# Kernel optimization log

Hardware: AMD Instinct MI355X
Metric: run time of the kernel (lower is better)

Reference implementation:

```python
import jax, jax.numpy as jnp
import numpy as np

B, S, H = 1024, 100, 256          # users(batch), seq_len, hidden
L, U = 20000, 20000               # location_size, user_size
EL, EU = 500000, 400000           # nnz of loc-loc and user-loc sparse graphs
LAMBDA_T, LAMBDA_S = 0.1, 1000.0
DAY = 86400.0


def setup_inputs() -> dict:
    key = jax.random.key(0)
    k = jax.random.split(key, 20)
    sd = 1.0 / np.sqrt(H)
    full_seq = jax.random.randint(k[0], (B, S), 0, L)
    full_seq_map = jax.random.randint(k[1], (B, S), 0, L)
    length = jax.random.randint(k[2], (B,), 1, S + 1)  # >=1 so mask never empty
    user_id = jax.random.randint(k[3], (B,), 0, U)
    time_delta = jax.random.uniform(k[4], (B, S), dtype=jnp.float32) * DAY
    geo_delta = jax.random.uniform(k[5], (B, S), dtype=jnp.float32) * 1e-3
    enc_emb = jax.random.normal(k[6], (L, H), dtype=jnp.float32) * sd
    user_emb = jax.random.normal(k[7], (U, H), dtype=jnp.float32) * sd
    emb2 = jax.random.normal(k[8], (L, H), dtype=jnp.float32) * sd  # embed_layer table
    # loc-loc random-walk graph (row-normalized weights), COO edge list
    row_loc = jax.random.randint(k[9], (EL,), 0, L)
    col_loc = jax.random.randint(k[10], (EL,), 0, L)
    vals_loc = jax.random.uniform(k[11], (EL,), dtype=jnp.float32) / (EL / L)
    # user-loc interact graph (row-normalized), COO edge list
    row_usr = jax.random.randint(k[12], (EU,), 0, U)
    col_usr = jax.random.randint(k[13], (EU,), 0, L)
    vals_usr = jax.random.uniform(k[14], (EU,), dtype=jnp.float32) / (EU / U)
    W_ih = jax.random.normal(k[15], (H, H), dtype=jnp.float32) * sd
    W_hh = jax.random.normal(k[16], (H, H), dtype=jnp.float32) * sd
    b_ih = jnp.zeros((H,), jnp.float32)
    b_hh = jnp.zeros((H,), jnp.float32)
    W1 = jax.random.normal(k[17], (L, 3 * H), dtype=jnp.float32) * sd  # source declares 2H but feeds 3H concat
    b1 = jnp.zeros((L,), jnp.float32)
    h0 = jax.random.normal(k[18], (B, H), dtype=jnp.float32) * (1.0 / H)  # per-user random init state
    return dict(full_seq=full_seq, full_seq_map=full_seq_map, length=length,
                user_id=user_id, time_delta=time_delta, geo_delta=geo_delta,
                enc_emb=enc_emb, user_emb=user_emb, emb2=emb2,
                row_loc=row_loc, col_loc=col_loc, vals_loc=vals_loc,
                row_usr=row_usr, col_usr=col_usr, vals_usr=vals_usr,
                W_ih=W_ih, W_hh=W_hh, b_ih=b_ih, b_hh=b_hh, W1=W1, b1=b1, h0=h0)


def reference(full_seq, full_seq_map, length, user_id, time_delta, geo_delta,
              enc_emb, user_emb, emb2, row_loc, col_loc, vals_loc,
              row_usr, col_usr, vals_usr, W_ih, W_hh, b_ih, b_hh, W1, b1, h0):
    # sparse.mm(graph, loc_emb): one random-walk propagation over locations
    encoder_weight = jax.ops.segment_sum(vals_loc[:, None] * enc_emb[col_loc],
                                         row_loc, num_segments=L)  # [L,H]
    x_emb = encoder_weight[full_seq_map]                           # [B,S,H]
    # sparse.mm(interact_graph, loc_emb): user preference from visited locations
    ew_user = jax.ops.segment_sum(vals_usr[:, None] * enc_emb[col_usr],
                                  row_usr, num_segments=U)         # [U,H]
    user_pref = ew_user[user_id][:, None, :]                       # [B,1,H]
    user_loc_sim = jnp.exp(-jnp.linalg.norm(user_pref - x_emb, axis=-1))  # [B,S]
    # vanilla tanh RNN (batch_first), scan over time
    def step(h, x_t):
        h = jnp.tanh(x_t @ W_ih.T + b_ih + h @ W_hh.T + b_hh)
        return h, h
    _, outs = jax.lax.scan(step, h0, jnp.swapaxes(x_emb, 0, 1))    # [S,B,H]
    out = jnp.swapaxes(outs, 0, 1)                                 # [B,S,H]
    # temporal / spatial decay weights
    a_j = (jnp.cos(time_delta * 2 * np.pi / DAY) + 1) / 2 * jnp.exp(-(time_delta / DAY * LAMBDA_T))
    b_j = jnp.exp(-geo_delta * LAMBDA_S)
    w_j = (a_j * b_j + 1e-10) * user_loc_sim
    mask = (length[:, None] > jnp.arange(S)[None, :]).astype(w_j.dtype)
    w_j = w_j * mask                                               # [B,S]
    denom = jnp.sum(w_j, axis=1, keepdims=True)                    # [B,1]
    out_w = jnp.sum(out * w_j[..., None], axis=1) / denom          # [B,H]
    x2 = emb2[full_seq]                                            # embed_layer (dropout=eval)
    out_w2 = jnp.sum(x2 * w_j[..., None], axis=1) / denom          # [B,H]
    p_u = user_emb[user_id]                                        # [B,H]
    feat = jnp.concatenate([out_w, p_u, out_w2], axis=1)           # [B,3H]
    return feat @ W1.T + b1                                        # [B,L]
```

## Files before the change

### kernel.cpp

```cpp
#include <hip/hip_runtime.h>
#include <math.h>

#define B_  1024
#define S_  100
#define H_  256
#define L_  20000
#define U_  20000
#define EL_ 500000
#define EU_ 400000

typedef __bf16 bf16x8 __attribute__((ext_vector_type(8)));
typedef __bf16 bf16x4 __attribute__((ext_vector_type(4)));
typedef float  f32x4  __attribute__((ext_vector_type(4)));
typedef _Float16 f16x8 __attribute__((ext_vector_type(8)));

__global__ void k_mark(const int* __restrict__ uid, int* __restrict__ flags) {
    int i = blockIdx.x * blockDim.x + threadIdx.x;
    if (i < B_) flags[uid[i]] = 1;
}

__global__ void k_hist2(const int* __restrict__ rowL, const int* __restrict__ rowU,
                        const int* __restrict__ flags,
                        int* __restrict__ cntL, int* __restrict__ cntU) {
    int e = blockIdx.x * blockDim.x + threadIdx.x;
    if (e < EL_) {
        atomicAdd(&cntL[rowL[e]], 1);
    } else if (e < EL_ + EU_) {
        int r = rowU[e - EL_];
        if (flags[r]) atomicAdd(&cntU[r], 1);
    }
}

__global__ __launch_bounds__(1024) void k_scan2(const int* __restrict__ cntA,
                                                int* __restrict__ offsA, int* __restrict__ curA,
                                                const int* __restrict__ cntB,
                                                int* __restrict__ offsB, int* __restrict__ curB) {
    const int* cnt = blockIdx.x ? cntB : cntA;
    int* offs      = blockIdx.x ? offsB : offsA;
    int* cursor    = blockIdx.x ? curB : curA;
    __shared__ int wsum[16];
    __shared__ int carry_s;
    int tid = threadIdx.x;
    int lane = tid & 63, wv = tid >> 6;
    if (tid == 0) carry_s = 0;
    __syncthreads();
    for (int base = 0; base < L_; base += 1024) {
        int v = (base + tid < L_) ? cnt[base + tid] : 0;
        int x = v;
#pragma unroll
        for (int off = 1; off < 64; off <<= 1) {
            int y = __shfl_up(x, off, 64);
            if (lane >= off) x += y;
        }
        if (lane == 63) wsum[wv] = x;
        __syncthreads();
        if (wv == 0) {
            int s = (lane < 16) ? wsum[lane] : 0;
#pragma unroll
            for (int off = 1; off < 16; off <<= 1) {
                int y = __shfl_up(s, off, 64);
                if (lane >= off) s += y;
            }
            if (lane < 16) wsum[lane] = s;
        }
        __syncthreads();
        int excl = x - v + (wv ? wsum[wv - 1] : 0) + carry_s;
        if (base + tid < L_) { offs[base + tid] = excl; cursor[base + tid] = excl; }
        __syncthreads();
        if (tid == 0) carry_s += wsum[15];
        __syncthreads();
    }
    if (tid == 0) offs[L_] = carry_s;
}

__global__ void k_place2(const int* __restrict__ rowL, const int* __restrict__ colL,
                         const float* __restrict__ valL, int* __restrict__ curL,
                         int* __restrict__ colLs, float* __restrict__ valLs,
                         const int* __restrict__ rowU, const int* __restrict__ colU,
                         const float* __restrict__ valU, const int* __restrict__ flags,
                         int* __restrict__ curU, int* __restrict__ colUs,
                         float* __restrict__ valUs) {
    int e = blockIdx.x * blockDim.x + threadIdx.x;
    if (e < EL_) {
        int pos = atomicAdd(&curL[rowL[e]], 1);
        colLs[pos] = colL[e];
        valLs[pos] = valL[e];
    } else if (e < EL_ + EU_) {
        int e2 = e - EL_;
        int r = rowU[e2];
        if (!flags[r]) return;
        int pos = atomicAdd(&curU[r], 1);
        colUs[pos] = colU[e2];
        valUs[pos] = valU[e2];
    }
}

__global__ __launch_bounds__(256) void k_gather2(
        const int* __restrict__ offsL, const int* __restrict__ colLs,
        const float* __restrict__ valLs, float* __restrict__ encw,
        const int* __restrict__ offsU, const int* __restrict__ colUs,
        const float* __restrict__ valUs, float* __restrict__ ewu,
        const int* __restrict__ flags, const float* __restrict__ emb) {
    int r = blockIdx.x;
    const int* offs; const int* col_s; const float* val_s; float* out;
    if (r < L_) {
        offs = offsL; col_s = colLs; val_s = valLs; out = encw;
    } else {
        r -= L_;
        if (!flags[r]) return;
        offs = offsU; col_s = colUs; val_s = valUs; out = ewu;
    }
    int tid = threadIdx.x;
    int lo = offs[r], hi = offs[r + 1];
    float acc = 0.f;
    int i = lo;
    for (; i + 1 < hi; i += 2) {
        int c0 = col_s[i], c1 = col_s[i + 1];
        float v0 = val_s[i], v1 = val_s[i + 1];
        float e0 = emb[(long long)c0 * H_ + tid];
        float e1 = emb[(long long)c1 * H_ + tid];
        acc += v0 * e0 + v1 * e1;
    }
    if (i < hi) acc += val_s[i] * emb[(long long)col_s[i] * H_ + tid];
    out[(long long)r * H_ + tid] = acc;
}

#define BM 128
#define BN 128
#define BK 16
#define PADW 132

__global__ __launch_bounds__(256) void k_gemm(
        const float* __restrict__ A, const float* __restrict__ Bm,
        const float* __restrict__ bias1, const float* __restrict__ bias2,
        float* __restrict__ C, int M, int N, int K) {
    __shared__ float As[BK][PADW];
    __shared__ float Bs[BK][PADW];
    int m0 = blockIdx.x * BM;
    int n0 = blockIdx.y * BN;
    int tid = threadIdx.x;
    int tn = tid & 15, tm = tid >> 4;

    float acc[8][8];
#pragma unroll
    for (int i = 0; i < 8; i++)
#pragma unroll
        for (int j = 0; j < 8; j++) acc[i][j] = 0.f;

    for (int k0 = 0; k0 < K; k0 += BK) {
#pragma unroll
        for (int h = 0; h < 2; h++) {
            int v = tid + h * 256;
            int rw = v >> 2, c4 = v & 3;
            int ar = m0 + rw; if (ar > M - 1) ar = M - 1;
            float4 a = *(const float4*)(A + (long long)ar * K + k0 + c4 * 4);
            As[c4 * 4 + 0][rw] = a.x; As[c4 * 4 + 1][rw] = a.y;
            As[c4 * 4 + 2][rw] = a.z; As[c4 * 4 + 3][rw] = a.w;
            int br = n0 + rw; if (br > N - 1) br = N - 1;
            float4 b = *(const float4*)(Bm + (long long)br * K + k0 + c4 * 4);
            Bs[c4 * 4 + 0][rw] = b.x; Bs[c4 * 4 + 1][rw] = b.y;
            Bs[c4 * 4 + 2][rw] = b.z; Bs[c4 * 4 + 3][rw] = b.w;
        }
        __syncthreads();
#pragma unroll
        for (int kk = 0; kk < BK; kk++) {
            float4 a0 = *(const float4*)&As[kk][tm * 8];
            float4 a1 = *(const float4*)&As[kk][tm * 8 + 4];
            float4 b0 = *(const float4*)&Bs[kk][tn * 8];
            float4 b1 = *(const float4*)&Bs[kk][tn * 8 + 4];
            float av[8] = {a0.x, a0.y, a0.z, a0.w, a1.x, a1.y, a1.z, a1.w};
            float bv[8] = {b0.x, b0.y, b0.z, b0.w, b1.x, b1.y, b1.z, b1.w};
#pragma unroll
            for (int i = 0; i < 8; i++)
#pragma unroll
                for (int j = 0; j < 8; j++) acc[i][j] += av[i] * bv[j];
        }
        __syncthreads();
    }

    float bsum[8];
#pragma unroll
    for (int j = 0; j < 8; j++) {
        int n = n0 + tn * 8 + j;
        float bb = 0.f;
        if (n < N) {
            if (bias1) bb += bias1[n];
            if (bias2) bb += bias2[n];
        }
        bsum[j] = bb;
    }
#pragma unroll
    for (int i = 0; i < 8; i++) {
        int m = m0 + tm * 8 + i;
        if (m < M) {
#pragma unroll
            for (int j = 0; j < 8; j++) {
                int n = n0 + tn * 8 + j;
                if (n < N) C[(long long)m * N + n] = acc[i][j] + bsum[j];
            }
        }
    }
}

__global__ __launch_bounds__(256) void k_cvt(const float4* __restrict__ src,
                                             bf16x4* __restrict__ dst, int n4) {
    int i = blockIdx.x * blockDim.x + threadIdx.x;
    if (i >= n4) return;
    float4 v = src[i];
    bf16x4 o;
    o[0] = (__bf16)v.x; o[1] = (__bf16)v.y; o[2] = (__bf16)v.z; o[3] = (__bf16)v.w;
    dst[i] = o;
}

__global__ __launch_bounds__(256) void k_gemm_bf16(
        const __bf16* __restrict__ A, const __bf16* __restrict__ Bw,
        const float* __restrict__ bias, float* __restrict__ C,
        int M, int N, int K) {
    __shared__ __bf16 Asl[128 * 32];
    __shared__ __bf16 Bsl[128 * 32];
    int tid = threadIdx.x;
    int lane = tid & 63, w = tid >> 6;
    int wm = w >> 1, wn = w & 1;
    int m0 = blockIdx.x * 128, n0 = blockIdx.y * 128;

    f32x4 acc[4][4];
#pragma unroll
    for (int i = 0; i < 4; i++)
#pragma unroll
        for (int j = 0; j < 4; j++) acc[i][j] = (f32x4){0.f, 0.f, 0.f, 0.f};

    int fm = lane & 15, fq = lane >> 4;

    for (int k0 = 0; k0 < K; k0 += 32) {
#pragma unroll
        for (int h = 0; h < 2; h++) {
            int c = h * 256 + w * 64 + lane;
            int r = c >> 2, qsw = c & 3;
            int q = qsw ^ ((r >> 1) & 3);
            const __bf16* gA = A + (long long)(m0 + r) * K + k0 + q * 8;
            __builtin_amdgcn_global_load_lds(
                (const __attribute__((address_space(1))) void*)gA,
                (__attribute__((address_space(3))) void*)(Asl + (h * 256 + w * 64) * 8),
                16, 0, 0);
            int br = n0 + r; if (br > N - 1) br = N - 1;
            const __bf16* gB = Bw + (long long)br * K + k0 + q * 8;
            __builtin_amdgcn_global_load_lds(
                (const __attribute__((address_space(1))) void*)gB,
                (__attribute__((address_space(3))) void*)(Bsl + (h * 256 + w * 64) * 8),
                16, 0, 0);
        }
        __syncthreads();

        bf16x8 af[4], bfr[4];
#pragma unroll
        for (int mi = 0; mi < 4; mi++) {
            int r = wm * 64 + mi * 16 + fm;
            int ch = r * 4 + (fq ^ ((r >> 1) & 3));
            af[mi] = *(const bf16x8*)(Asl + ch * 8);
        }
#pragma unroll
        for (int ni = 0; ni < 4; ni++) {
            int r = wn * 64 + ni * 16 + fm;
            int ch = r * 4 + (fq ^ ((r >> 1) & 3));
            bfr[ni] = *(const bf16x8*)(Bsl + ch * 8);
        }
#pragma unroll
        for (int mi = 0; mi < 4; mi++)
#pragma unroll
            for (int ni = 0; ni < 4; ni++)
                acc[mi][ni] = __builtin_amdgcn_mfma_f32_16x16x32_bf16(
                    af[mi], bfr[ni], acc[mi][ni], 0, 0, 0);
        __syncthreads();
    }

#pragma unroll
    for (int ni = 0; ni < 4; ni++) {
        int col = n0 + wn * 64 + ni * 16 + fm;
        if (col >= N) continue;
        float bb = bias[col];
#pragma unroll
        for (int mi = 0; mi < 4; mi++) {
            int row = m0 + wm * 64 + mi * 16 + fq * 4;
#pragma unroll
            for (int r = 0; r < 4; r++)
                C[(long long)(row + r) * N + col] = acc[mi][ni][r] + bb;
        }
    }
}

__global__ __launch_bounds__(256) void k_simwj(
        const int* __restrict__ map, const int* __restrict__ length, const int* __restrict__ uid,
        const float* __restrict__ td_, const float* __restrict__ gd_,
        const float* __restrict__ encw, const float* __restrict__ ewu,
        float* __restrict__ wj, float* __restrict__ denom) {
    int b = blockIdx.x;
    __shared__ float up[H_];
    __shared__ float wjl[S_];
    int tid = threadIdx.x;
    int u = uid[b];
    up[tid] = ewu[(long long)u * H_ + tid];
    __syncthreads();
    int wv = tid >> 6, lane = tid & 63;
    int len = length[b];
    for (int s = wv; s < S_; s += 4) {
        int mi = map[b * S_ + s];
        float4 x = ((const float4*)(encw + (long long)mi * H_))[lane];
        float4 uu = *(const float4*)&up[lane * 4];
        float dx = uu.x - x.x, dy = uu.y - x.y, dz = uu.z - x.z, dw = uu.w - x.w;
        float d2 = dx * dx + dy * dy + dz * dz + dw * dw;
#pragma unroll
        for (int off = 32; off; off >>= 1) d2 += __shfl_xor(d2, off, 64);
        if (lane == 0) {
            float nrm = sqrtf(d2);
            float sim = expf(-nrm);
            float td = td_[b * S_ + s], gd = gd_[b * S_ + s];
            float aj = (cosf(td * 7.27220521664304e-05f) + 1.0f) * 0.5f *
                       expf(-td * 1.1574074074074073e-06f);
            float bj = expf(-gd * 1000.0f);
            float w = (aj * bj + 1e-10f) * sim;
            if (s >= len) w = 0.f;
            wjl[s] = w;
            wj[b * S_ + s] = w;
        }
    }
    __syncthreads();
    if (tid < 64) {
        float v = (tid < S_) ? wjl[tid] : 0.f;
        if (tid + 64 < S_) v += wjl[tid + 64];
#pragma unroll
        for (int off = 32; off; off >>= 1) v += __shfl_xor(v, off, 64);
        if (tid == 0) denom[b] = v;
    }
}

#define RNN_STRIDE 264

__global__ __launch_bounds__(512, 1) void k_rnn_mfma(
        const float* __restrict__ EWW, const float* __restrict__ Whh,
        const int* __restrict__ map, const float* __restrict__ wj,
        const float* __restrict__ h0g, float* __restrict__ out_acc) {
    __shared__ _Float16 hbuf[16 * RNN_STRIDE];
    __shared__ int   maps_s[S_ * 16];
    __shared__ float wjs_s[S_ * 16];

    int tid = threadIdx.x;
    int lane = tid & 63, w = tid >> 6;
    int fm = lane & 15, fq = lane >> 4;
    int b0 = blockIdx.x * 16;

    for (int i = tid; i < 16 * S_; i += 512) {
        int m = i / S_, s = i - m * S_;
        maps_s[s * 16 + m] = map[(b0 + m) * S_ + s];
        wjs_s[s * 16 + m] = wj[(b0 + m) * S_ + s];
    }
    if (tid < 256) {
        int m = tid >> 4, seg = tid & 15;
        const float4* src = (const float4*)(h0g + (long long)(b0 + m) * H_ + seg * 16);
        float4 a = src[0], bq = src[1], cq = src[2], dq = src[3];
        f16x8 v0, v1;
        v0[0] = (_Float16)a.x;  v0[1] = (_Float16)a.y;  v0[2] = (_Float16)a.z;  v0[3] = (_Float16)a.w;
        v0[4] = (_Float16)bq.x; v0[5] = (_Float16)bq.y; v0[6] = (_Float16)bq.z; v0[7] = (_Float16)bq.w;
        v1[0] = (_Float16)cq.x; v1[1] = (_Float16)cq.y; v1[2] = (_Float16)cq.z; v1[3] = (_Float16)cq.w;
        v1[4] = (_Float16)dq.x; v1[5] = (_Float16)dq.y; v1[6] = (_Float16)dq.z; v1[7] = (_Float16)dq.w;
        *(f16x8*)(hbuf + m * RNN_STRIDE + seg * 16) = v0;
        *(f16x8*)(hbuf + m * RNN_STRIDE + seg * 16 + 8) = v1;
    }

    f16x8 wf[2][8];
#pragma unroll
    for (int ni = 0; ni < 2; ni++) {
        const float* wrow = Whh + (long long)(w * 32 + ni * 16 + fm) * H_;
#pragma unroll
        for (int c = 0; c < 8; c++) {
            int k = c * 32 + fq * 8;
            float4 p = *(const float4*)(wrow + k);
            float4 q = *(const float4*)(wrow + k + 4);
            f16x8 v;
            v[0] = (_Float16)p.x; v[1] = (_Float16)p.y; v[2] = (_Float16)p.z; v[3] = (_Float16)p.w;
            v[4] = (_Float16)q.x; v[5] = (_Float16)q.y; v[6] = (_Float16)q.z; v[7] = (_Float16)q.w;
            wf[ni][c] = v;
        }
    }

    float accv[2][4];
#pragma unroll
    for (int ni = 0; ni < 2; ni++)
#pragma unroll
        for (int r = 0; r < 4; r++) accv[ni][r] = 0.f;

    __syncthreads();

    float xc[2][4], xn[2][4];
#pragma unroll
    for (int r = 0; r < 4; r++) {
        const float* xp = EWW + (long long)maps_s[0 * 16 + fq * 4 + r] * H_;
#pragma unroll
        for (int ni = 0; ni < 2; ni++) xc[ni][r] = xp[w * 32 + ni * 16 + fm];
    }

    for (int s = 0; s < S_; s++) {
        f32x4 acc[2];
#pragma unroll
        for (int ni = 0; ni < 2; ni++)
            acc[ni] = (f32x4){xc[ni][0], xc[ni][1], xc[ni][2], xc[ni][3]};

        if (s + 1 < S_) {
#pragma unroll
            for (int r = 0; r < 4; r++) {
                const float* xp = EWW + (long long)maps_s[(s + 1) * 16 + fq * 4 + r] * H_;
#pragma unroll
                for (int ni = 0; ni < 2; ni++) xn[ni][r] = xp[w * 32 + ni * 16 + fm];
            }
        }

        f16x8 af[8];
#pragma unroll
        for (int c = 0; c < 8; c++)
            af[c] = *(const f16x8*)(hbuf + fm * RNN_STRIDE + c * 32 + fq * 8);
#pragma unroll
        for (int c = 0; c < 8; c++)
#pragma unroll
            for (int ni = 0; ni < 2; ni++)
                acc[ni] = __builtin_amdgcn_mfma_f32_16x16x32_f16(af[c], wf[ni][c], acc[ni], 0, 0, 0);
        __syncthreads();

        float wjr[4];
#pragma unroll
        for (int r = 0; r < 4; r++) wjr[r] = wjs_s[s * 16 + fq * 4 + r];
#pragma unroll
        for (int ni = 0; ni < 2; ni++) {
#pragma unroll
            for (int r = 0; r < 4; r++) {
                float t = acc[ni][r];
                t = fminf(15.f, fmaxf(-15.f, t));
                float e = __expf(2.f * t);
                float hv = 1.f - 2.f / (e + 1.f);
                accv[ni][r] += wjr[r] * hv;
                hbuf[(fq * 4 + r) * RNN_STRIDE + w * 32 + ni * 16 + fm] = (_Float16)hv;
            }
        }
        __syncthreads();

#pragma unroll
        for (int ni = 0; ni < 2; ni++)
#pragma unroll
            for (int r = 0; r < 4; r++) xc[ni][r] = xn[ni][r];
    }

#pragma unroll
    for (int ni = 0; ni < 2; ni++)
#pragma unroll
        for (int r = 0; r < 4; r++)
            out_acc[(long long)(b0 + fq * 4 + r) * H_ + w * 32 + ni * 16 + fm] = accv[ni][r];
}

__global__ __launch_bounds__(256) void k_feat(
        const float* __restrict__ out_acc, const float* __restrict__ denom,
        const int* __restrict__ uid, const float* __restrict__ user_emb,
        const int* __restrict__ seq, const float* __restrict__ wj,
        const float* __restrict__ emb2, float* __restrict__ feat) {
    int b = blockIdx.x, j = threadIdx.x;
    __shared__ float wjl[S_];
    __shared__ int sq[S_];
    if (j < S_) {
        wjl[j] = wj[b * S_ + j];
        sq[j] = seq[b * S_ + j];
    }
    __syncthreads();
    float inv = 1.f / denom[b];
    feat[(long long)b * 768 + j] = out_acc[(long long)b * H_ + j] * inv;
    feat[(long long)b * 768 + 256 + j] = user_emb[(long long)uid[b] * H_ + j];
    float a2 = 0.f;
    for (int s = 0; s < S_; s++) a2 += wjl[s] * emb2[(long long)sq[s] * H_ + j];
    feat[(long long)b * 768 + 512 + j] = a2 * inv;
}

extern "C" void kernel_launch(void* const* d_in, const int* in_sizes, int n_in,
                              void* d_out, int out_size, void* d_ws, size_t ws_size,
                              hipStream_t stream) {
    const int*   full_seq     = (const int*)d_in[0];
    const int*   full_seq_map = (const int*)d_in[1];
    const int*   length       = (const int*)d_in[2];
    const int*   user_id      = (const int*)d_in[3];
    const float* time_delta   = (const float*)d_in[4];
    const float* geo_delta    = (const float*)d_in[5];
    const float* enc_emb      = (const float*)d_in[6];
    const float* user_emb     = (const float*)d_in[7];
    const float* emb2         = (const float*)d_in[8];
    const int*   row_loc      = (const int*)d_in[9];
    const int*   col_loc      = (const int*)d_in[10];
    const float* vals_loc     = (const float*)d_in[11];
    const int*   row_usr      = (const int*)d_in[12];
    const int*   col_usr      = (const int*)d_in[13];
    const float* vals_usr     = (const float*)d_in[14];
    const float* W_ih         = (const float*)d_in[15];
    const float* W_hh         = (const float*)d_in[16];
    const float* b_ih         = (const float*)d_in[17];
    const float* b_hh         = (const float*)d_in[18];
    const float* W1           = (const float*)d_in[19];
    const float* b1           = (const float*)d_in[20];
    const float* h0g          = (const float*)d_in[21];
    float* out = (float*)d_out;

    float* ws = (float*)d_ws;
    size_t o = 0;
    int*   flags = (int*)(ws + o); o += U_;
    float* ewu   = ws + o; o += (size_t)U_ * H_;
    float* encw  = ws + o; o += (size_t)L_ * H_;
    float* EWW   = ws + o; o += (size_t)L_ * H_;
    size_t late_base = o;
    float* wj    = ws + o; o += (size_t)B_ * S_;
    float* denom = ws + o; o += B_;
    float* oacc  = ws + o; o += (size_t)B_ * H_;
    float* feat  = ws + o; o += (size_t)B_ * 3 * H_;
    size_t a = late_base;
    int*   cntL  = (int*)(ws + a); a += L_ + 1;
    int*   offsL = (int*)(ws + a); a += L_ + 1;
    int*   curL  = (int*)(ws + a); a += L_ + 1;
    int*   colLs = (int*)(ws + a); a += EL_;
    float* valLs = ws + a;         a += EL_;
    int*   cntU  = (int*)EWW;
    int*   offsU = cntU + (U_ + 1);
    int*   curU  = offsU + (U_ + 1);
    int*   colUs = curU + (U_ + 1);
    float* valUs = (float*)(colUs + EU_);
    __bf16* w1bf   = (__bf16*)ws;
    __bf16* featbf = (__bf16*)EWW;

    hipMemsetAsync(flags, 0, U_ * sizeof(int), stream);
    hipMemsetAsync(cntL, 0, (L_ + 1) * sizeof(int), stream);
    hipMemsetAsync(cntU, 0, (U_ + 1) * sizeof(int), stream);
    k_mark<<<(B_ + 255) / 256, 256, 0, stream>>>(user_id, flags);

    k_hist2<<<(EL_ + EU_ + 255) / 256, 256, 0, stream>>>(row_loc, row_usr, flags, cntL, cntU);
    k_scan2<<<2, 1024, 0, stream>>>(cntL, offsL, curL, cntU, offsU, curU);
    k_place2<<<(EL_ + EU_ + 255) / 256, 256, 0, stream>>>(
        row_loc, col_loc, vals_loc, curL, colLs, valLs,
        row_usr, col_usr, vals_usr, flags, curU, colUs, valUs);
    k_gather2<<<L_ + U_, 256, 0, stream>>>(offsL, colLs, valLs, encw,
                                           offsU, colUs, valUs, ewu, flags, enc_emb);

    k_gemm<<<dim3((L_ + BM - 1) / BM, (H_ + BN - 1) / BN), 256, 0, stream>>>(
        encw, W_ih, b_ih, b_hh, EWW, L_, H_, H_);
    k_simwj<<<B_, 256, 0, stream>>>(full_seq_map, length, user_id, time_delta,
                                    geo_delta, encw, ewu, wj, denom);
    k_rnn_mfma<<<B_ / 16, 512, 0, stream>>>(EWW, W_hh, full_seq_map, wj, h0g, oacc);
    k_feat<<<B_, 256, 0, stream>>>(oacc, denom, user_id, user_emb, full_seq, wj, emb2, feat);

    k_cvt<<<((L_ * 3 * H_ / 4) + 255) / 256, 256, 0, stream>>>(
        (const float4*)W1, (bf16x4*)w1bf, L_ * 3 * H_ / 4);
    k_cvt<<<((B_ * 3 * H_ / 4) + 255) / 256, 256, 0, stream>>>(
        (const float4*)feat, (bf16x4*)featbf, B_ * 3 * H_ / 4);

    k_gemm_bf16<<<dim3(B_ / 128, (L_ + 127) / 128), 256, 0, stream>>>(
        featbf, w1bf, b1, out, B_, L_, 3 * H_);
}
```

Baseline: 678.2 us.

## Prefetch RNN input rows into LDS with async global_load_lds triple buffering

Replaces the per-lane register prefetch of projected input rows in the recurrent kernel with asynchronous global-to-LDS loads, using a three-slot LDS ring and a prefetch distance of two steps. Barriers become manual s_waitcnt plus s_barrier so each step waits only for the slot it is about to read. The goal is to hide gather latency on the serial recurrence's critical path and to cut scattered per-lane global loads. It adds 48KB of LDS and depends on hand-written waitcnt ordering being correct.

```diff
diff --git a/kernel.cpp b/kernel.cpp
--- a/kernel.cpp
+++ b/kernel.cpp
@@ -340,6 +340,7 @@
         const int* __restrict__ map, const float* __restrict__ wj,
         const float* __restrict__ h0g, float* __restrict__ out_acc) {
     __shared__ _Float16 hbuf[16 * RNN_STRIDE];
+    __shared__ float    Xbuf[3][16 * H_];
     __shared__ int   maps_s[S_ * 16];
     __shared__ float wjs_s[S_ * 16];
 
@@ -390,39 +391,69 @@
 
     __syncthreads();
 
-    float xc[2][4], xn[2][4];
-#pragma unroll
-    for (int r = 0; r < 4; r++) {
-        const float* xp = EWW + (long long)maps_s[0 * 16 + fq * 4 + r] * H_;
-#pragma unroll
-        for (int ni = 0; ni < 2; ni++) xc[ni][r] = xp[w * 32 + ni * 16 + fm];
-    }
-
+    {
+        int r0 = maps_s[0 * 16 + w];
+        __builtin_amdgcn_global_load_lds(
+            (const __attribute__((address_space(1))) void*)(EWW + (long long)r0 * H_ + lane * 4),
+            (__attribute__((address_space(3))) void*)(&Xbuf[0][w * H_]), 16, 0, 0);
+        int r1 = maps_s[0 * 16 + 8 + w];
+        __builtin_amdgcn_global_load_lds(
+            (const __attribute__((address_space(1))) void*)(EWW + (long long)r1 * H_ + lane * 4),
+            (__attribute__((address_space(3))) void*)(&Xbuf[0][(8 + w) * H_]), 16, 0, 0);
+        int r2 = maps_s[1 * 16 + w];
+        __builtin_amdgcn_global_load_lds(
+            (const __attribute__((address_space(1))) void*)(EWW + (long long)r2 * H_ + lane * 4),
+            (__attribute__((address_space(3))) void*)(&Xbuf[1][w * H_]), 16, 0, 0);
+        int r3 = maps_s[1 * 16 + 8 + w];
+        __builtin_amdgcn_global_load_lds(
+            (const __attribute__((address_space(1))) void*)(EWW + (long long)r3 * H_ + lane * 4),
+            (__attribute__((address_space(3))) void*)(&Xbuf[1][(8 + w) * H_]), 16, 0, 0);
+    }
+    asm volatile("s_waitcnt vmcnt(2)" ::: "memory");
+    __builtin_amdgcn_sched_barrier(0);
+    __builtin_amdgcn_s_barrier();
+
+    int xb = 0;
     for (int s = 0; s < S_; s++) {
+        int xb2 = xb + 2; if (xb2 >= 3) xb2 -= 3;
+
+        if (s + 2 < S_) {
+            int r0 = maps_s[(s + 2) * 16 + w];
+            __builtin_amdgcn_global_load_lds(
+                (const __attribute__((address_space(1))) void*)(EWW + (long long)r0 * H_ + lane * 4),
+                (__attribute__((address_space(3))) void*)(&Xbuf[xb2][w * H_]), 16, 0, 0);
+            int r1 = maps_s[(s + 2) * 16 + 8 + w];
+            __builtin_amdgcn_global_load_lds(
+                (const __attribute__((address_space(1))) void*)(EWW + (long long)r1 * H_ + lane * 4),
+                (__attribute__((address_space(3))) void*)(&Xbuf[xb2][(8 + w) * H_]), 16, 0, 0);
+        }
+
+        float xc[2][4];
+#pragma unroll
+        for (int r = 0; r < 4; r++) {
+            const float* xrow = &Xbuf[xb][(fq * 4 + r) * H_];
+            xc[0][r] = xrow[w * 32 + fm];
+            xc[1][r] = xrow[w * 32 + 16 + fm];
+        }
+
+        f16x8 af[8];
+#pragma unroll
+        for (int c = 0; c < 8; c++)
+            af[c] = *(const f16x8*)(hbuf + fm * RNN_STRIDE + c * 32 + fq * 8);
+
         f32x4 acc[2];
 #pragma unroll
         for (int ni = 0; ni < 2; ni++)
             acc[ni] = (f32x4){xc[ni][0], xc[ni][1], xc[ni][2], xc[ni][3]};
-
-        if (s + 1 < S_) {
-#pragma unroll
-            for (int r = 0; r < 4; r++) {
-                const float* xp = EWW + (long long)maps_s[(s + 1) * 16 + fq * 4 + r] * H_;
-#pragma unroll
-                for (int ni = 0; ni < 2; ni++) xn[ni][r] = xp[w * 32 + ni * 16 + fm];
-            }
-        }
-
-        f16x8 af[8];
-#pragma unroll
-        for (int c = 0; c < 8; c++)
-            af[c] = *(const f16x8*)(hbuf + fm * RNN_STRIDE + c * 32 + fq * 8);
 #pragma unroll
         for (int c = 0; c < 8; c++)
 #pragma unroll
             for (int ni = 0; ni < 2; ni++)
                 acc[ni] = __builtin_amdgcn_mfma_f32_16x16x32_f16(af[c], wf[ni][c], acc[ni], 0, 0, 0);
-        __syncthreads();
+
+        asm volatile("s_waitcnt lgkmcnt(0)" ::: "memory");
+        __builtin_amdgcn_sched_barrier(0);
+        __builtin_amdgcn_s_barrier();
 
         float wjr[4];
 #pragma unroll
@@ -439,12 +470,17 @@
                 hbuf[(fq * 4 + r) * RNN_STRIDE + w * 32 + ni * 16 + fm] = (_Float16)hv;
             }
         }
-        __syncthreads();
-
-#pragma unroll
-        for (int ni = 0; ni < 2; ni++)
-#pragma unroll
-            for (int r = 0; r < 4; r++) xc[ni][r] = xn[ni][r];
+
+        asm volatile("s_waitcnt lgkmcnt(0)" ::: "memory");
+        if (s + 2 < S_) {
+            asm volatile("s_waitcnt vmcnt(2)" ::: "memory");
+        } else {
+            asm volatile("s_waitcnt vmcnt(0)" ::: "memory");
+        }
+        __builtin_amdgcn_sched_barrier(0);
+        __builtin_amdgcn_s_barrier();
+
+        xb = xb + 1; if (xb >= 3) xb -= 3;
     }
 
 #pragma unroll
```

Result: slower. 715.6 us (+5.5%).
